# Optimization experiments

Measured on AMD Instinct MI355X. Metric: run time of the kernel, lower is better.

## Reference

```python
import jax, jax.numpy as jnp
import numpy as np

N = 50000        # nodes
E = 800000       # edges (avg degree 16)
HID = 96         # hidden_channels
HEADS = 4        # heads passed to SRGATConv
D = HID // HEADS # per-head dim
R = 38           # num_relations
NEG_SLOPE = 0.2  # LeakyReLU slope for attention logits


def setup_inputs() -> dict:
    key = jax.random.key(0)
    ks = jax.random.split(key, 9)
    x = jax.random.normal(ks[0], (N, HID), jnp.float32)
    edge_index = jax.random.randint(ks[1], (2, E), 0, N, dtype=jnp.int32)
    edge_type = jax.random.randint(ks[2], (E,), 0, R, dtype=jnp.int32)
    s = 1.0 / np.sqrt(HID)
    W = jax.random.normal(ks[3], (HID, HID), jnp.float32) * s          # node projection
    rel_emb = jax.random.normal(ks[4], (R, HID), jnp.float32) * s      # relation embeddings
    att_src = jax.random.normal(ks[5], (HEADS, D), jnp.float32) * 0.1  # attention vectors
    att_dst = jax.random.normal(ks[6], (HEADS, D), jnp.float32) * 0.1
    att_rel = jax.random.normal(ks[7], (HEADS, D), jnp.float32) * 0.1
    bias = jnp.zeros((HID,), jnp.float32)
    return {"x": x, "edge_index": edge_index, "edge_type": edge_type,
            "W": W, "rel_emb": rel_emb, "att_src": att_src,
            "att_dst": att_dst, "att_rel": att_rel, "bias": bias}


def reference(x, edge_index, edge_type, W, rel_emb, att_src, att_dst, att_rel, bias):
    # SRGATConv: relation-aware multi-head graph attention, then GELU wrapper.
    n = x.shape[0]
    src, dst = edge_index[0], edge_index[1]
    h = (x @ W).reshape(n, HEADS, D)                    # [N,H,D]
    r = rel_emb[edge_type].reshape(-1, HEADS, D)        # [E,H,D] gathered relation feats
    h_src = h[src]                                      # [E,H,D] irregular gather
    h_dst = h[dst]
    # attention logits per edge/head
    logits = ((h_src * att_src).sum(-1)
              + (h_dst * att_dst).sum(-1)
              + (r * att_rel).sum(-1))                  # [E,H]
    logits = jax.nn.leaky_relu(logits, NEG_SLOPE)
    # segment softmax over incoming edges of each destination node
    lmax = jax.ops.segment_max(logits, dst, num_segments=n)   # [N,H]
    e = jnp.exp(logits - lmax[dst])
    denom = jax.ops.segment_sum(e, dst, num_segments=n)       # [N,H]
    alpha = e / denom[dst]                                    # [E,H]
    # weighted message scatter
    msg = alpha[:, :, None] * (h_src + r)                     # [E,H,D]
    out = jax.ops.segment_sum(msg, dst, num_segments=n).reshape(n, HID) + bias
    out = jax.nn.gelu(out)
    return out, alpha
```

## Files before the change

kernel.cpp:

```cpp
#include <hip/hip_runtime.h>
#include <hip/hip_fp16.h>
#include <math.h>

#define HIDC 96
#define HEADS 4
#define RMAX 40
#define BINSZ 64
#define BINB 6
#define BINCAP 1344
#define TILE 2048
#define SRCB 18
#define SRCM ((1 << SRCB) - 1)
#define ETB 6
#define NBMAX 1024

typedef unsigned u32x2 __attribute__((ext_vector_type(2)));
typedef _Float16 f16x4 __attribute__((ext_vector_type(4)));
typedef float f32x4 __attribute__((ext_vector_type(4)));

__device__ __forceinline__ __half2 u2h2(unsigned u) {
    return *reinterpret_cast<__half2*>(&u);
}
__device__ __forceinline__ unsigned h22u(__half2 h) {
    return *reinterpret_cast<unsigned*>(&h);
}

__global__ __launch_bounds__(256) void gemm96(
    const float* __restrict__ x, const float* __restrict__ W,
    const float* __restrict__ att_src, const float* __restrict__ att_dst,
    const float* __restrict__ rel, const float* __restrict__ att_rel,
    __half* __restrict__ h16, float4* __restrict__ ps,
    float* __restrict__ pdi, float4* __restrict__ pr,
    int* __restrict__ bincnt, int4* __restrict__ csrtail,
    int n, int nbins, int R_) {
    for (int i = blockIdx.x * 256 + threadIdx.x; i < nbins; i += gridDim.x * 256)
        bincnt[i] = 0;
    if (blockIdx.x == 0 && threadIdx.x < 16)
        csrtail[threadIdx.x] = make_int4(0, 0, 0, 0);
    if (blockIdx.x == 0 && threadIdx.x < R_) {
        int t = threadIdx.x;
        const float4* rp = reinterpret_cast<const float4*>(rel + (size_t)t * HIDC);
        const float4* ar = reinterpret_cast<const float4*>(att_rel);
        float acc[HEADS] = {0, 0, 0, 0};
#pragma unroll
        for (int c = 0; c < 24; ++c) {
            float4 v = rp[c], a = ar[c];
            acc[c / 6] += v.x * a.x + v.y * a.y + v.z * a.z + v.w * a.w;
        }
        pr[t] = make_float4(acc[0], acc[1], acc[2], acc[3]);
    }

    const int lane = threadIdx.x & 63;
    const int wave = threadIdx.x >> 6;
    const int lo16 = lane & 15;
    const int grp = lane >> 4;

    f16x4 bf[6][6];
#pragma unroll
    for (int kf = 0; kf < 6; ++kf)
#pragma unroll
        for (int nt = 0; nt < 6; ++nt) {
            f16x4 b;
#pragma unroll
            for (int j = 0; j < 4; ++j)
                b[j] = (_Float16)W[(kf * 16 + grp * 4 + j) * HIDC + nt * 16 + lo16];
            bf[kf][nt] = b;
        }

    int row0 = blockIdx.x * 64 + wave * 16;
    if (row0 >= n) return;
    int r = row0 + lo16;
    const float4* xr = reinterpret_cast<const float4*>(
        x + (size_t)min(r, n - 1) * HIDC);

    f32x4 c[6];
#pragma unroll
    for (int nt = 0; nt < 6; ++nt) c[nt] = (f32x4){0.f, 0.f, 0.f, 0.f};

#pragma unroll
    for (int kf = 0; kf < 6; ++kf) {
        float4 av = xr[kf * 4 + grp];
        f16x4 af;
        af[0] = (_Float16)av.x; af[1] = (_Float16)av.y;
        af[2] = (_Float16)av.z; af[3] = (_Float16)av.w;
#pragma unroll
        for (int nt = 0; nt < 6; ++nt)
            c[nt] = __builtin_amdgcn_mfma_f32_16x16x16f16(af, bf[kf][nt], c[nt], 0, 0, 0);
    }

#pragma unroll
    for (int nt = 0; nt < 6; ++nt)
#pragma unroll
        for (int i = 0; i < 4; ++i) {
            int rr = row0 + grp * 4 + i;
            if (rr < n)
                h16[(size_t)rr * HIDC + nt * 16 + lo16] = (__half)c[nt][i];
        }

    float as_[6], ad_[6];
#pragma unroll
    for (int nt = 0; nt < 6; ++nt) {
        as_[nt] = att_src[nt * 16 + lo16];
        ad_[nt] = att_dst[nt * 16 + lo16];
    }
    bool lo8 = lo16 < 8;
    float a1lo = lo8 ? as_[1] : 0.f, a1hi = lo8 ? 0.f : as_[1];
    float d1lo = lo8 ? ad_[1] : 0.f, d1hi = lo8 ? 0.f : ad_[1];
    float a4lo = lo8 ? as_[4] : 0.f, a4hi = lo8 ? 0.f : as_[4];
    float d4lo = lo8 ? ad_[4] : 0.f, d4hi = lo8 ? 0.f : ad_[4];

    float sA[4][4], sD[4][4];
#pragma unroll
    for (int i = 0; i < 4; ++i) {
        float v0 = c[0][i], v1 = c[1][i], v2 = c[2][i];
        float v3 = c[3][i], v4 = c[4][i], v5 = c[5][i];
        sA[i][0] = v0 * as_[0] + v1 * a1lo;
        sA[i][1] = v1 * a1hi + v2 * as_[2];
        sA[i][2] = v3 * as_[3] + v4 * a4lo;
        sA[i][3] = v4 * a4hi + v5 * as_[5];
        sD[i][0] = v0 * ad_[0] + v1 * d1lo;
        sD[i][1] = v1 * d1hi + v2 * ad_[2];
        sD[i][2] = v3 * ad_[3] + v4 * d4lo;
        sD[i][3] = v4 * d4hi + v5 * ad_[5];
    }
#pragma unroll
    for (int i = 0; i < 4; ++i)
#pragma unroll
        for (int h = 0; h < 4; ++h) {
#pragma unroll
            for (int m = 1; m < 16; m <<= 1) {
                sA[i][h] += __shfl_xor(sA[i][h], m);
                sD[i][h] += __shfl_xor(sD[i][h], m);
            }
        }
    {
        int rr = row0 + grp * 4 + lo16;
        if (lo16 < 4 && rr < n) {
            float4 pv, dv;
            if (lo16 == 0) {
                pv = make_float4(sA[0][0], sA[0][1], sA[0][2], sA[0][3]);
                dv = make_float4(sD[0][0], sD[0][1], sD[0][2], sD[0][3]);
            } else if (lo16 == 1) {
                pv = make_float4(sA[1][0], sA[1][1], sA[1][2], sA[1][3]);
                dv = make_float4(sD[1][0], sD[1][1], sD[1][2], sD[1][3]);
            } else if (lo16 == 2) {
                pv = make_float4(sA[2][0], sA[2][1], sA[2][2], sA[2][3]);
                dv = make_float4(sD[2][0], sD[2][1], sD[2][2], sD[2][3]);
            } else {
                pv = make_float4(sA[3][0], sA[3][1], sA[3][2], sA[3][3]);
                dv = make_float4(sD[3][0], sD[3][1], sD[3][2], sD[3][3]);
            }
            ps[rr] = pv;
            *reinterpret_cast<float4*>(pdi + (size_t)rr * 8) = dv;
        }
    }
}

__device__ __forceinline__ float4 ev4(float4 a, float4 b, float4 c) {
    float l0 = a.x + b.x + c.x, l1 = a.y + b.y + c.y;
    float l2 = a.z + b.z + c.z, l3 = a.w + b.w + c.w;
    l0 = l0 >= 0.f ? l0 : 0.2f * l0;
    l1 = l1 >= 0.f ? l1 : 0.2f * l1;
    l2 = l2 >= 0.f ? l2 : 0.2f * l2;
    l3 = l3 >= 0.f ? l3 : 0.2f * l3;
    return make_float4(__expf(l0), __expf(l1), __expf(l2), __expf(l3));
}

__device__ __forceinline__ float gelu_f(float v) {
    float u = 0.7978845608028654f * (v + 0.044715f * v * v * v);
    u = fminf(fmaxf(u, -15.f), 15.f);
    float t = __expf(2.f * u);
    return 0.5f * v * (1.f + (t - 1.f) / (t + 1.f));
}

__global__ __launch_bounds__(256) void bin_edges(
    const int* __restrict__ src, const int* __restrict__ dst,
    const int* __restrict__ et,
    int* __restrict__ bincnt, int2* __restrict__ binwords,
    int E_, int nbins) {
    __shared__ int hist[NBMAX];
    __shared__ int base[NBMAX];
    int e0 = blockIdx.x * TILE;
    for (int i = threadIdx.x; i < nbins; i += 256) hist[i] = 0;
    __syncthreads();
    int mybin[8], myrank[8], myword[8];
#pragma unroll
    for (int u = 0; u < 8; ++u) {
        int e = e0 + u * 256 + threadIdx.x;
        mybin[u] = -1;
        if (e < E_) {
            int d = dst[e];
            int b = d >> BINB;
            myword[u] = src[e] | (et[e] << SRCB) | ((d & (BINSZ - 1)) << (SRCB + ETB));
            mybin[u] = b;
            myrank[u] = atomicAdd(&hist[b], 1);
        }
    }
    __syncthreads();
    for (int i = threadIdx.x; i < nbins; i += 256)
        base[i] = hist[i] > 0 ? atomicAdd(&bincnt[i], hist[i]) : 0;
    __syncthreads();
#pragma unroll
    for (int u = 0; u < 8; ++u) {
        if (mybin[u] >= 0) {
            int pos = base[mybin[u]] + myrank[u];
            if (pos < BINCAP)
                binwords[(size_t)mybin[u] * BINCAP + pos] =
                    make_int2(myword[u], e0 + u * 256 + threadIdx.x);
        }
    }
}

__global__ __launch_bounds__(256) void bin_sort(
    const int* __restrict__ bincnt, const int2* __restrict__ binwords,
    const float4* __restrict__ ps, const float* __restrict__ pdi,
    const float4* __restrict__ prg,
    int4* __restrict__ csr, int* __restrict__ noff, int* __restrict__ ncnt,
    int n, int R_) {
    __shared__ int cnts[BINSZ];
    __shared__ int scanb[BINSZ];
    __shared__ int nbase[BINSZ];
    __shared__ float4 pdl[BINSZ];
    __shared__ float4 prl[RMAX];
    int bin = blockIdx.x;
    int node0 = bin * BINSZ;
    int total = min(bincnt[bin], BINCAP);

    for (int i = threadIdx.x; i < BINSZ; i += 256) {
        cnts[i] = 0;
        int nd = node0 + i;
        pdl[i] = (nd < n) ? *reinterpret_cast<const float4*>(pdi + (size_t)nd * 8)
                          : make_float4(0.f, 0.f, 0.f, 0.f);
    }
    for (int i = threadIdx.x; i < R_; i += 256) prl[i] = prg[i];
    __syncthreads();

    int2 w[6];
    int rk[6];
    float4 psv[6];
#pragma unroll
    for (int u = 0; u < 6; ++u) {
        int k = u * 256 + threadIdx.x;
        rk[u] = -1;
        if (k < total) {
            w[u] = binwords[(size_t)bin * BINCAP + k];
            psv[u] = ps[w[u].x & SRCM];
            int dl = (w[u].x >> (SRCB + ETB)) & (BINSZ - 1);
            rk[u] = atomicAdd(&cnts[dl], 1);
        }
    }
    __syncthreads();

    if (threadIdx.x < 64) {
        int v = (cnts[threadIdx.x] + 3) & ~3;
#pragma unroll
        for (int s = 1; s < 64; s <<= 1) {
            int t = __shfl_up(v, s, 64);
            if ((int)threadIdx.x >= s) v += t;
        }
        scanb[threadIdx.x] = v;
    }
    __syncthreads();
    if (threadIdx.x < BINSZ) {
        int cnt = cnts[threadIdx.x];
        int cntP = (cnt + 3) & ~3;
        int nb = scanb[threadIdx.x] - cntP;
        nbase[threadIdx.x] = nb;
        int nd = node0 + threadIdx.x;
        if (nd < n) {
            noff[nd] = bin * BINCAP + nb;
            ncnt[nd] = cnt;
        }
        int4 z = make_int4(0, 0, 0, 0);
        for (int i = cnt; i < cntP; ++i)
            csr[(size_t)bin * BINCAP + nb + i] = z;
    }
    {
        int gt = scanb[BINSZ - 1];
        if (threadIdx.x < 12) {
            int p = gt + threadIdx.x;
            if (p < BINCAP)
                csr[(size_t)bin * BINCAP + p] = make_int4(0, 0, 0, 0);
        }
    }
    __syncthreads();

#pragma unroll
    for (int u = 0; u < 6; ++u) {
        if (rk[u] >= 0) {
            int s = w[u].x & SRCM;
            int t = (w[u].x >> SRCB) & ((1 << ETB) - 1);
            int dl = (w[u].x >> (SRCB + ETB)) & (BINSZ - 1);
            unsigned e = (unsigned)w[u].y;
            float4 v = ev4(psv[u], pdl[dl], prl[t]);
            int4 pk;
            pk.x = (int)((unsigned)(s * (HIDC * 2)) | ((e & 0xFFu) << 24));
            pk.y = (int)((unsigned)(t * (HIDC * 2)) | ((e >> 8) << 13));
            pk.z = (int)h22u(__floats2half2_rn(v.x, v.y));
            pk.w = (int)h22u(__floats2half2_rn(v.z, v.w));
            csr[(size_t)bin * BINCAP + nbase[dl] + rk[u]] = pk;
        }
    }
}

__global__ __launch_bounds__(256) void node_agg(
    const __half* __restrict__ h16, const float* __restrict__ rel,
    const int4* __restrict__ csr, const int* __restrict__ noff,
    const int* __restrict__ ncnt,
    const float* __restrict__ bias,
    float* __restrict__ out, float4* __restrict__ alpha, int n, int R_) {
    __shared__ uint2 relh[RMAX * HIDC / 4];
    for (int i = threadIdx.x; i < R_ * 24; i += 256) {
        float4 v = reinterpret_cast<const float4*>(rel)[i];
        uint2 pk;
        pk.x = h22u(__floats2half2_rn(v.x, v.y));
        pk.y = h22u(__floats2half2_rn(v.z, v.w));
        relh[i] = pk;
    }
    __syncthreads();

    int lane = threadIdx.x & 31;
    if (lane >= 24) return;
    const int j = lane;
    const int j4 = 4 * j;
    const int hh = j / 6;
    const unsigned joff = (unsigned)(j << 3);
    const float4 bv = *reinterpret_cast<const float4*>(bias + j4);
    const char* h16c = reinterpret_cast<const char*>(h16);
    const char* relc = reinterpret_cast<const char*>(relh);
    const unsigned esel = (unsigned)(2 * hh) | ((unsigned)(2 * hh + 1) << 8);

    int hw0 = (blockIdx.x * blockDim.x + threadIdx.x) >> 5;
    int nHW = (gridDim.x * blockDim.x) >> 5;

    for (int hw = hw0; hw < n; hw += nHW) {
        int cnt = ncnt[hw];
        const int4* sp0 = csr + noff[hw];
        const int4* sp = sp0;
        float a0 = 0.f, a1 = 0.f, a2 = 0.f, a3 = 0.f;
        float dsum = 0.f;

        if (cnt > 0) {
            int cntP = (cnt + 3) & ~3;
            int4 pc[4];
#pragma unroll
            for (int u = 0; u < 4; ++u) pc[u] = sp[u];
            sp += 4;

            for (int k = 0; k < cntP; k += 4, sp += 4) {
                uint2 hv[4], rv[4];
#pragma unroll
                for (int u = 0; u < 4; ++u)
                    hv[u] = *reinterpret_cast<const uint2*>(
                        h16c + ((unsigned)pc[u].x & 0x00FFFFFFu) + joff);
#pragma unroll
                for (int u = 0; u < 4; ++u)
                    rv[u] = *reinterpret_cast<const uint2*>(
                        relc + ((unsigned)pc[u].y & 0x1FFFu) + joff);
                int4 pn[4];
#pragma unroll
                for (int u = 0; u < 4; ++u) pn[u] = sp[u];
#pragma unroll
                for (int u = 0; u < 4; ++u) {
                    unsigned e32 = __builtin_amdgcn_perm(
                        (unsigned)pc[u].w, (unsigned)pc[u].z, esel);
                    dsum += __half2float(__low2half(u2h2(e32)));
                    unsigned s01 = h22u(__hadd2(u2h2(hv[u].x), u2h2(rv[u].x)));
                    unsigned s23 = h22u(__hadd2(u2h2(hv[u].y), u2h2(rv[u].y)));
                    asm("v_fma_mix_f32 %0, %1, %2, %0 op_sel:[0,0,0] op_sel_hi:[1,1,0]"
                        : "+v"(a0) : "v"(s01), "v"(e32));
                    asm("v_fma_mix_f32 %0, %1, %2, %0 op_sel:[1,0,0] op_sel_hi:[1,1,0]"
                        : "+v"(a1) : "v"(s01), "v"(e32));
                    asm("v_fma_mix_f32 %0, %1, %2, %0 op_sel:[0,0,0] op_sel_hi:[1,1,0]"
                        : "+v"(a2) : "v"(s23), "v"(e32));
                    asm("v_fma_mix_f32 %0, %1, %2, %0 op_sel:[1,0,0] op_sel_hi:[1,1,0]"
                        : "+v"(a3) : "v"(s23), "v"(e32));
                }
#pragma unroll
                for (int u = 0; u < 4; ++u) pc[u] = pn[u];
            }
        }
        float inv = dsum > 0.f ? 1.f / dsum : 0.f;
        float4 o;
        o.x = gelu_f(a0 * inv + bv.x);
        o.y = gelu_f(a1 * inv + bv.y);
        o.z = gelu_f(a2 * inv + bv.z);
        o.w = gelu_f(a3 * inv + bv.w);
        *reinterpret_cast<float4*>(out + (size_t)hw * HIDC + j4) = o;

        if (cnt > 0) {
            float iv0 = __shfl(inv, 0, 32);
            float iv1 = __shfl(inv, 6, 32);
            float iv2 = __shfl(inv, 12, 32);
            float iv3 = __shfl(inv, 18, 32);
            for (int k = j; k < cnt; k += 24) {
                int4 pk = sp0[k];
                unsigned e_id = ((unsigned)pk.x >> 24) | (((unsigned)pk.y >> 13) << 8);
                float2 f01 = __half22float2(u2h2((unsigned)pk.z));
                float2 f23 = __half22float2(u2h2((unsigned)pk.w));
                alpha[e_id] = make_float4(f01.x * iv0, f01.y * iv1,
                                          f23.x * iv2, f23.y * iv3);
            }
        }
    }
}

extern "C" void kernel_launch(void* const* d_in, const int* in_sizes, int n_in,
                              void* d_out, int out_size, void* d_ws, size_t ws_size,
                              hipStream_t stream) {
    const float* x       = (const float*)d_in[0];
    const int*   eidx    = (const int*)d_in[1];
    const int*   etype   = (const int*)d_in[2];
    const float* W       = (const float*)d_in[3];
    const float* rel     = (const float*)d_in[4];
    const float* att_src = (const float*)d_in[5];
    const float* att_dst = (const float*)d_in[6];
    const float* att_rel = (const float*)d_in[7];
    const float* bias    = (const float*)d_in[8];

    int N_ = in_sizes[0] / HIDC;
    int E_ = in_sizes[1] / 2;
    int R_ = in_sizes[4] / HIDC;
    const int* src  = eidx;
    const int* dstp = eidx + E_;
    int nbins = (N_ + BINSZ - 1) / BINSZ;

    char* ws = (char*)d_ws;
    __half* h16      = (__half*)ws; ws += (size_t)N_ * HIDC * 2;
    float4* ps       = (float4*)ws; ws += (size_t)N_ * 16;
    float*  pdi      = (float*)ws;  ws += (size_t)N_ * 32;
    float4* pr       = (float4*)ws; ws += 1024;
    int*    bincnt   = (int*)ws;    ws += (size_t)((nbins + 3) & ~3) * 4;
    int*    noff     = (int*)ws;    ws += (size_t)((N_ + 3) & ~3) * 4;
    int*    ncnt     = (int*)ws;    ws += (size_t)((N_ + 3) & ~3) * 4;
    int2*   binwords = (int2*)ws;   ws += (size_t)nbins * BINCAP * 8;
    int4*   csr      = (int4*)ws;   ws += (size_t)nbins * BINCAP * 16 + 256;

    float*  outv  = (float*)d_out;
    float4* alpha = (float4*)(outv + (size_t)N_ * HIDC);

    gemm96<<<(N_ + 63) / 64, 256, 0, stream>>>(
        x, W, att_src, att_dst, rel, att_rel, h16, ps, pdi, pr,
        bincnt, csr + (size_t)nbins * BINCAP, N_, nbins, R_);

    bin_edges<<<(E_ + TILE - 1) / TILE, 256, 0, stream>>>(
        src, dstp, etype, bincnt, binwords, E_, nbins);

    bin_sort<<<nbins, 256, 0, stream>>>(
        bincnt, binwords, ps, pdi, pr, csr, noff, ncnt, N_, R_);

    node_agg<<<(N_ + 15) / 16, 256, 0, stream>>>(
        h16, rel, csr, noff, ncnt, bias, outv, alpha, N_, R_);
}
```

Baseline: 172.8 us.

## Merge GEMM and edge-binning kernels into one heterogeneous launch

Fuses the node projection GEMM and the edge binning pass into a single kernel, where blocks beyond the GEMM range run the binning logic. Because the two stages are independent, they can overlap on the GPU, and one launch boundary goes away. Zeroing of the bin counters and the CSR tail moves to hipMemsetAsync calls ahead of the launch, since binning blocks can no longer depend on the GEMM blocks to clear them. The memsets add two small stream operations, and the fused kernel's register and LDS footprint is now the maximum of both paths, which may lower occupancy.

```diff
diff --git a/kernel.cpp b/kernel.cpp
--- a/kernel.cpp
+++ b/kernel.cpp
@@ -25,18 +25,54 @@
     return *reinterpret_cast<unsigned*>(&h);
 }
 
-__global__ __launch_bounds__(256) void gemm96(
+__global__ __launch_bounds__(256) void gemm_bin(
     const float* __restrict__ x, const float* __restrict__ W,
     const float* __restrict__ att_src, const float* __restrict__ att_dst,
     const float* __restrict__ rel, const float* __restrict__ att_rel,
     __half* __restrict__ h16, float4* __restrict__ ps,
     float* __restrict__ pdi, float4* __restrict__ pr,
-    int* __restrict__ bincnt, int4* __restrict__ csrtail,
-    int n, int nbins, int R_) {
-    for (int i = blockIdx.x * 256 + threadIdx.x; i < nbins; i += gridDim.x * 256)
-        bincnt[i] = 0;
-    if (blockIdx.x == 0 && threadIdx.x < 16)
-        csrtail[threadIdx.x] = make_int4(0, 0, 0, 0);
+    const int* __restrict__ srcp, const int* __restrict__ dstp,
+    const int* __restrict__ etp,
+    int* __restrict__ bincnt, int2* __restrict__ binwords,
+    int n, int nbins, int R_, int E_, int gemmBlocks) {
+
+    if ((int)blockIdx.x >= gemmBlocks) {
+        __shared__ int hist[NBMAX];
+        __shared__ int base[NBMAX];
+        int bid = blockIdx.x - gemmBlocks;
+        int e0 = bid * TILE;
+        for (int i = threadIdx.x; i < nbins; i += 256) hist[i] = 0;
+        __syncthreads();
+        int mybin[8], myrank[8], myword[8];
+#pragma unroll
+        for (int u = 0; u < 8; ++u) {
+            int e = e0 + u * 256 + threadIdx.x;
+            mybin[u] = -1;
+            if (e < E_) {
+                int d = dstp[e];
+                int b = d >> BINB;
+                myword[u] = srcp[e] | (etp[e] << SRCB) |
+                            ((d & (BINSZ - 1)) << (SRCB + ETB));
+                mybin[u] = b;
+                myrank[u] = atomicAdd(&hist[b], 1);
+            }
+        }
+        __syncthreads();
+        for (int i = threadIdx.x; i < nbins; i += 256)
+            base[i] = hist[i] > 0 ? atomicAdd(&bincnt[i], hist[i]) : 0;
+        __syncthreads();
+#pragma unroll
+        for (int u = 0; u < 8; ++u) {
+            if (mybin[u] >= 0) {
+                int pos = base[mybin[u]] + myrank[u];
+                if (pos < BINCAP)
+                    binwords[(size_t)mybin[u] * BINCAP + pos] =
+                        make_int2(myword[u], e0 + u * 256 + threadIdx.x);
+            }
+        }
+        return;
+    }
+
     if (blockIdx.x == 0 && threadIdx.x < R_) {
         int t = threadIdx.x;
         const float4* rp = reinterpret_cast<const float4*>(rel + (size_t)t * HIDC);
@@ -173,44 +209,6 @@
     return 0.5f * v * (1.f + (t - 1.f) / (t + 1.f));
 }
 
-__global__ __launch_bounds__(256) void bin_edges(
-    const int* __restrict__ src, const int* __restrict__ dst,
-    const int* __restrict__ et,
-    int* __restrict__ bincnt, int2* __restrict__ binwords,
-    int E_, int nbins) {
-    __shared__ int hist[NBMAX];
-    __shared__ int base[NBMAX];
-    int e0 = blockIdx.x * TILE;
-    for (int i = threadIdx.x; i < nbins; i += 256) hist[i] = 0;
-    __syncthreads();
-    int mybin[8], myrank[8], myword[8];
-#pragma unroll
-    for (int u = 0; u < 8; ++u) {
-        int e = e0 + u * 256 + threadIdx.x;
-        mybin[u] = -1;
-        if (e < E_) {
-            int d = dst[e];
-            int b = d >> BINB;
-            myword[u] = src[e] | (et[e] << SRCB) | ((d & (BINSZ - 1)) << (SRCB + ETB));
-            mybin[u] = b;
-            myrank[u] = atomicAdd(&hist[b], 1);
-        }
-    }
-    __syncthreads();
-    for (int i = threadIdx.x; i < nbins; i += 256)
-        base[i] = hist[i] > 0 ? atomicAdd(&bincnt[i], hist[i]) : 0;
-    __syncthreads();
-#pragma unroll
-    for (int u = 0; u < 8; ++u) {
-        if (mybin[u] >= 0) {
-            int pos = base[mybin[u]] + myrank[u];
-            if (pos < BINCAP)
-                binwords[(size_t)mybin[u] * BINCAP + pos] =
-                    make_int2(myword[u], e0 + u * 256 + threadIdx.x);
-        }
-    }
-}
-
 __global__ __launch_bounds__(256) void bin_sort(
     const int* __restrict__ bincnt, const int2* __restrict__ binwords,
     const float4* __restrict__ ps, const float* __restrict__ pdi,
@@ -439,12 +437,15 @@
     float*  outv  = (float*)d_out;
     float4* alpha = (float4*)(outv + (size_t)N_ * HIDC);
 
-    gemm96<<<(N_ + 63) / 64, 256, 0, stream>>>(
+    int gemmBlocks = (N_ + 63) / 64;
+    int edgeBlocks = (E_ + TILE - 1) / TILE;
+
+    hipMemsetAsync(bincnt, 0, (size_t)nbins * 4, stream);
+    hipMemsetAsync(csr + (size_t)nbins * BINCAP, 0, 16 * sizeof(int4), stream);
+
+    gemm_bin<<<gemmBlocks + edgeBlocks, 256, 0, stream>>>(
         x, W, att_src, att_dst, rel, att_rel, h16, ps, pdi, pr,
-        bincnt, csr + (size_t)nbins * BINCAP, N_, nbins, R_);
-
-    bin_edges<<<(E_ + TILE - 1) / TILE, 256, 0, stream>>>(
-        src, dstp, etype, bincnt, binwords, E_, nbins);
+        src, dstp, etype, bincnt, binwords, N_, nbins, R_, E_, gemmBlocks);
 
     bin_sort<<<nbins, 256, 0, stream>>>(
         bincnt, binwords, ps, pdi, pr, csr, noff, ncnt, N_, R_);
```

Result: no change. 172.5 us (-0.2%).
